# Performance work log

Hardware: AMD Instinct MI355X
Metric: run time of the kernel (lower is better)

Reference implementation:

```python
import jax, jax.numpy as jnp
import numpy as np


def setup_inputs() -> dict:
    key = jax.random.key(0)
    ks = jax.random.split(key, 6)
    B, C, V, L = 64, 32, 512, 13
    C_OUT = 64
    C_CAT = (2 * 3 + 1) * C  # order*support_len + 1 = 7 blocks -> 224
    x = jax.random.normal(ks[0], (B, C, V, L), dtype=jnp.float32)
    support0 = jax.random.uniform(ks[1], (V, V), dtype=jnp.float32)
    support1 = jax.random.uniform(ks[2], (V, V), dtype=jnp.float32)
    support2 = jax.random.uniform(ks[3], (V, V), dtype=jnp.float32)
    W = jax.random.normal(ks[4], (C_OUT, C_CAT), dtype=jnp.float32) * 0.05
    b = jnp.zeros((C_OUT,), dtype=jnp.float32)
    return {"x": x, "support0": support0, "support1": support1,
            "support2": support2, "W": W, "b": b}


def reference(x, support0, support1, support2, W, b):
    # Graph WaveNet GCN, eval mode (dropout is identity at inference).
    # x: [B, C, V, L]; each support a: [V, V].
    outs = [x]
    for a in (support0, support1, support2):
        x1 = jnp.einsum('ncvl,vw->ncwl', x, a)   # order 1 propagation
        outs.append(x1)
        x2 = jnp.einsum('ncvl,vw->ncwl', x1, a)  # order 2 propagation
        outs.append(x2)
    h = jnp.concatenate(outs, axis=1)            # [B, 7*C, V, L]
    # 1x1 Conv2d == per-(v,l) linear over channels
    h = jnp.einsum('ncvl,oc->novl', h, W) + b[None, :, None, None]
    return h
```

## Files before the change

kernel.cpp:

```cpp
#include <hip/hip_runtime.h>


typedef unsigned short u16;
typedef unsigned int   u32;
typedef __bf16 bf16x8 __attribute__((ext_vector_type(8)));
typedef float  f32x4  __attribute__((ext_vector_type(4)));
typedef u16    u16x4  __attribute__((ext_vector_type(4)));
typedef u16    u16x8  __attribute__((ext_vector_type(8)));

#define DEVI static __device__ __forceinline__

#define NV   512
#define NL   13
#define SZA  262144L
#define YP   136
#define WP   232

#define VMCNT(n) asm volatile("s_waitcnt vmcnt(" #n ")" ::: "memory")
#define LGKM0    asm volatile("s_waitcnt lgkmcnt(0)" ::: "memory")
#define CFENCE   asm volatile("" ::: "memory")
#define BAR()    __builtin_amdgcn_s_barrier()

DEVI u16 f2bf(float f) {
  union { float f; u32 u; } v; v.f = f;
  u32 u = v.u;
  return (u16)((u + 0x7fffu + ((u >> 16) & 1u)) >> 16);
}

DEVI void gl2lds16(const void* g, void* l) {
  __builtin_amdgcn_global_load_lds((__attribute__((address_space(1))) void*)g,
                                   (__attribute__((address_space(3))) void*)l, 16, 0, 0);
}

__global__ __launch_bounds__(256) void prep_A(const float* __restrict__ A0,
                                              const float* __restrict__ A1,
                                              const float* __restrict__ A2,
                                              u16* __restrict__ BT,
                                              u16* __restrict__ ABF) {
  const int s = blockIdx.z;
  const float* A = (s == 0) ? A0 : ((s == 1) ? A1 : A2);
  u16* abf = ABF + (long)s * SZA;
  u16* bt  = BT + (long)(2 * s) * SZA;
  __shared__ float t[32][33];
  const int v0 = blockIdx.x * 32, w0 = blockIdx.y * 32;
  const int tid = threadIdx.x;
  for (int i = tid; i < 1024; i += 256) {
    const int r = i >> 5, c = i & 31;
    const float val = A[(long)(v0 + r) * 512 + w0 + c];
    t[r][c] = val;
    abf[(long)(v0 + r) * 512 + w0 + c] = f2bf(val);
  }
  __syncthreads();
  for (int i = tid; i < 1024; i += 256) {
    const int r = i >> 5, c = i & 31;
    bt[(long)(w0 + r) * 512 + v0 + c] = f2bf(t[c][r]);
  }
}

__global__ __launch_bounds__(256) void prep_W(const float* __restrict__ W,
                                              u16* __restrict__ WBF) {
  const int i = blockIdx.x * 256 + threadIdx.x;
  WBF[i] = f2bf(W[i]);
}

__global__ __launch_bounds__(256) void transpose_x(const float* __restrict__ x,
                                                   u16* __restrict__ XT) {
  __shared__ __align__(16) float tile[NV * NL];
  const int bc = blockIdx.x;
  const int b = bc >> 5, c = bc & 31;
  const float4* src4 = (const float4*)(x + (long)bc * (NV * NL));
  float4* t4 = (float4*)tile;
  for (int i = threadIdx.x; i < (NV * NL) / 4; i += 256) t4[i] = src4[i];
  __syncthreads();
  for (int j = threadIdx.x; j < NL * 256; j += 256) {
    const int l = j >> 8, v = (j & 255) * 2;
    const long row = (long)(b * 13 + l) * 32 + c;
    const u32 lo = f2bf(tile[v * NL + l]);
    const u32 hi = f2bf(tile[(v + 1) * NL + l]);
    *(u32*)&XT[row * 512 + v] = lo | (hi << 16);
  }
}

__global__ __launch_bounds__(256) void gemm512(const u16* __restrict__ Ag,
                                               const u16* __restrict__ Bg,
                                               u16* __restrict__ Cg,
                                               long aZ, long bZ, long cZ) {
  __shared__ __align__(16) u16 As[128 * 32];
  __shared__ __align__(16) u16 Bs[128 * 32];
  const int p = blockIdx.z;
  const u16* A = Ag + (long)p * aZ;
  const u16* B = Bg + (long)p * bZ;
  u16*       C = Cg + (long)p * cZ;
  const int m0 = blockIdx.y * 128, n0 = blockIdx.x * 128;
  const int tid = threadIdx.x;
  const int lane = tid & 63, wid = tid >> 6;
  const int wm = wid >> 1, wn = wid & 1;
  const int lr = lane & 15, lq = lane >> 4;
  const int srow = lane >> 2, skq = lane & 3;

  f32x4 acc[4][4] = {};

  for (int kt = 0; kt < 16; ++kt) {
    const int k0 = kt * 32;
    __syncthreads();
#pragma unroll
    for (int j = 0; j < 2; ++j) {
      const int rb = wid * 32 + j * 16;
      gl2lds16(A + (long)(m0 + rb + srow) * 512 + (k0 + skq * 8), &As[rb * 32]);
      gl2lds16(B + (long)(n0 + rb + srow) * 512 + (k0 + skq * 8), &Bs[rb * 32]);
    }
    __syncthreads();
    bf16x8 af[4], bv[4];
#pragma unroll
    for (int t = 0; t < 4; ++t) {
      af[t] = *(const bf16x8*)&As[(wm * 64 + t * 16 + lr) * 32 + lq * 8];
      bv[t] = *(const bf16x8*)&Bs[(wn * 64 + t * 16 + lr) * 32 + lq * 8];
    }
#pragma unroll
    for (int i = 0; i < 4; ++i)
#pragma unroll
      for (int j = 0; j < 4; ++j)
        acc[i][j] = __builtin_amdgcn_mfma_f32_16x16x32_bf16(af[i], bv[j], acc[i][j], 0, 0, 0);
  }
#pragma unroll
  for (int i = 0; i < 4; ++i) {
    const int mr = m0 + wm * 64 + i * 16 + lq * 4;
#pragma unroll
    for (int j = 0; j < 4; ++j) {
      const int nc = n0 + wn * 64 + j * 16 + lr;
#pragma unroll
      for (int r = 0; r < 4; ++r)
        C[(long)(mr + r) * 512 + nc] = f2bf(acc[i][j][r]);
    }
  }
}

__global__ __launch_bounds__(512) void fused_gcn(const u16* __restrict__ XT,
                                                 const u16* __restrict__ BT,
                                                 const u16* __restrict__ WBF,
                                                 const float* __restrict__ bias,
                                                 float* __restrict__ out) {
  __shared__ __align__(16) u16 As [3][128 * 32];
  __shared__ __align__(16) u16 Bs0[3][128 * 32];
  __shared__ __align__(16) u16 Bs1[3][128 * 32];
  __shared__ __align__(16) u16 Yt[128 * YP];
  __shared__ __align__(16) u16 Ws[64 * WP];

  const int P = blockIdx.x;
  const int xcd = P & 7, inner = P >> 3;
  const int ym = xcd * 26 + (inner >> 2);
  const int m0 = ym * 128;
  const int w0 = (inner & 3) * 128;

  const int tid  = threadIdx.x;
  const int lane = tid & 63, wid = tid >> 6;
  const int lr = lane & 15, lq = lane >> 4;
  const int ww = wid & 3, wm2 = wid >> 2;
  const int g  = wid >> 1, h  = wid & 1;
  const int srow = tid >> 2, skq = tid & 3;
  const int scol = (skq ^ ((srow >> 1) & 3)) * 8;
  const int ldsb = wid * 512;
  const int co = (lq ^ ((lr >> 1) & 3)) * 8;

  for (int i = tid; i < 64 * 56; i += 512) {
    const int row = i / 56, c4 = (i - row * 56) * 4;
    *(u16x4*)&Ws[row * WP + c4] = *(const u16x4*)&WBF[row * 224 + c4];
  }
  for (int i = tid; i < 2048; i += 512) {
    const int mrow = i >> 4, c8 = (i & 15) * 8;
    const u16x8 d = *(const u16x8*)&XT[(long)(m0 + mrow) * 512 + w0 + c8];
#pragma unroll
    for (int z = 0; z < 8; ++z) {
      const int w = c8 + z;
      Yt[w * YP + ((((mrow >> 3) ^ ((w >> 3) & 3)) << 3) | (mrow & 7))] = d[z];
    }
  }
  __syncthreads();

  f32x4 oacc[4][4] = {};

#define STAGE(Bp0_, Bp1_, kk, bb) do {                                         \
    const int kc_ = (kk) * 32 + scol;                                          \
    gl2lds16(XT     + (long)(m0 + srow) * 512 + kc_, &As [bb][ldsb]);          \
    gl2lds16((Bp0_) + (long)(w0 + srow) * 512 + kc_, &Bs0[bb][ldsb]);          \
    gl2lds16((Bp1_) + (long)(w0 + srow) * 512 + kc_, &Bs1[bb][ldsb]);          \
  } while (0)

#define PROJ(blk) do {                                                         \
    bf16x8 paf_[4], pbv_[4];                                                   \
    _Pragma("unroll")                                                          \
    for (int oi = 0; oi < 4; ++oi)                                             \
      paf_[oi] = *(const bf16x8*)&Ws[(oi * 16 + lr) * WP + (blk) * 32 + lq * 8]; \
    _Pragma("unroll")                                                          \
    for (int wj = 0; wj < 4; ++wj) {                                           \
      const int w_ = h * 64 + wj * 16 + lr;                                    \
      pbv_[wj] = *(const bf16x8*)&Yt[w_ * YP + (((g * 4 + lq) ^ ((w_ >> 3) & 3)) << 3)]; \
    }                                                                          \
    _Pragma("unroll")                                                          \
    for (int oi = 0; oi < 4; ++oi)                                             \
      _Pragma("unroll")                                                        \
      for (int wj = 0; wj < 4; ++wj)                                           \
        oacc[oi][wj] = __builtin_amdgcn_mfma_f32_16x16x32_bf16(paf_[oi], pbv_[wj], oacc[oi][wj], 0, 0, 0); \
  } while (0)

#define WRB(ac) do {                                                           \
    _Pragma("unroll")                                                          \
    for (int i = 0; i < 2; ++i)                                                \
      _Pragma("unroll")                                                        \
      for (int j = 0; j < 4; ++j)                                              \
        _Pragma("unroll")                                                      \
        for (int r = 0; r < 4; ++r) {                                          \
          const int w_ = ww * 32 + i * 16 + lq * 4 + r;                        \
          const int m_ = wm2 * 64 + j * 16 + lr;                               \
          Yt[w_ * YP + ((((m_ >> 3) ^ ((w_ >> 3) & 3)) << 3) | (m_ & 7))] = f2bf(ac[i][j][r]); \
        }                                                                      \
  } while (0)

  for (int pass = 0; pass < 3; ++pass) {
    const u16* Bp0 = BT + (long)(2 * pass) * SZA;
    const u16* Bp1 = BT + (long)(2 * pass + 1) * SZA;
    STAGE(Bp0, Bp1, 0, 0);
    STAGE(Bp0, Bp1, 1, 1);
    PROJ(2 * pass);
    f32x4 accA[2][4] = {}, accB[2][4] = {};
#pragma unroll
    for (int kt = 0; kt < 16; ++kt) {
      if (kt == 15) { VMCNT(0); } else { VMCNT(3); }
      BAR();
      CFENCE;
      if (kt < 14) STAGE(Bp0, Bp1, kt + 2, (kt + 2) % 3);
      const int buf = kt % 3;
      bf16x8 a0[2], a1[2], bv[4];
#pragma unroll
      for (int i = 0; i < 2; ++i) {
        a0[i] = *(const bf16x8*)&Bs0[buf][(ww * 32 + i * 16 + lr) * 32 + co];
        a1[i] = *(const bf16x8*)&Bs1[buf][(ww * 32 + i * 16 + lr) * 32 + co];
      }
#pragma unroll
      for (int j = 0; j < 4; ++j)
        bv[j] = *(const bf16x8*)&As[buf][(wm2 * 64 + j * 16 + lr) * 32 + co];
      LGKM0;
#pragma unroll
      for (int i = 0; i < 2; ++i)
#pragma unroll
        for (int j = 0; j < 4; ++j) {
          accA[i][j] = __builtin_amdgcn_mfma_f32_16x16x32_bf16(a0[i], bv[j], accA[i][j], 0, 0, 0);
          accB[i][j] = __builtin_amdgcn_mfma_f32_16x16x32_bf16(a1[i], bv[j], accB[i][j], 0, 0, 0);
        }
    }
    WRB(accA);  LGKM0; BAR(); CFENCE;
    PROJ(2 * pass + 1);  LGKM0; BAR(); CFENCE;
    WRB(accB);  LGKM0; BAR(); CFENCE;
  }
  PROJ(6);

  const int bl = ym * 4 + g;
  const int b  = bl / 13, l = bl - b * 13;
  float* outb = out + (long)b * (64L * 512 * 13) + l;
#pragma unroll
  for (int oi = 0; oi < 4; ++oi) {
    const f32x4 bi = *(const f32x4*)&bias[oi * 16 + lq * 4];
#pragma unroll
    for (int wj = 0; wj < 4; ++wj) {
      const int w = w0 + h * 64 + wj * 16 + lr;
      const long base = ((long)(oi * 16 + lq * 4) * 512 + w) * 13;
#pragma unroll
      for (int r = 0; r < 4; ++r)
        outb[base + (long)r * (512 * 13)] = oacc[oi][wj][r] + bi[r];
    }
  }
#undef STAGE
#undef PROJ
#undef WRB
}

extern "C" void kernel_launch(void* const* d_in, const int* in_sizes, int n_in,
                              void* d_out, int out_size, void* d_ws, size_t ws_size,
                              hipStream_t stream) {
  const float* x  = (const float*)d_in[0];
  const float* s0 = (const float*)d_in[1];
  const float* s1 = (const float*)d_in[2];
  const float* s2 = (const float*)d_in[3];
  const float* W  = (const float*)d_in[4];
  const float* b  = (const float*)d_in[5];
  float* out = (float*)d_out;

  char* ws = (char*)d_ws;
  u16* XT  = (u16*)(ws);
  u16* BT  = (u16*)(ws + 27262976L);
  u16* ABF = (u16*)(ws + 30408704L);
  u16* WBF = (u16*)(ws + 31981568L);

  prep_A<<<dim3(16, 16, 3), 256, 0, stream>>>(s0, s1, s2, BT, ABF);
  prep_W<<<dim3(56), 256, 0, stream>>>(W, WBF);
  gemm512<<<dim3(4, 4, 3), 256, 0, stream>>>(BT, ABF, BT + SZA,
                                             2L * SZA, 1L * SZA, 2L * SZA);
  transpose_x<<<dim3(64 * 32), 256, 0, stream>>>(x, XT);
  fused_gcn<<<dim3(832), 512, 0, stream>>>(XT, BT, WBF, b, out);
}
```

Baseline: 419.8 us.

## Merge prep kernels and halve fused GCN tile for two blocks per CU

Merges the x transpose, support conversion and W conversion into a single prep launch, which removes two kernel launches. The fused GCN kernel now uses 256-thread blocks with 64-wide w tiles, launch_bounds(256,2) and a smaller LDS footprint so two blocks can share a CU. The W projection fragments are loaded from global memory into registers instead of being staged in LDS, and sched_barriers are added around the pipeline stages. In exchange, the grid is twice as large, so each support tile of XT is re-read by more blocks and register pressure rises.

```diff
diff --git a/kernel.cpp b/kernel.cpp
--- a/kernel.cpp
+++ b/kernel.cpp
@@ -5,7 +5,6 @@
 typedef unsigned int   u32;
 typedef __bf16 bf16x8 __attribute__((ext_vector_type(8)));
 typedef float  f32x4  __attribute__((ext_vector_type(4)));
-typedef u16    u16x4  __attribute__((ext_vector_type(4)));
 typedef u16    u16x8  __attribute__((ext_vector_type(8)));
 
 #define DEVI static __device__ __forceinline__
@@ -13,13 +12,11 @@
 #define NV   512
 #define NL   13
 #define SZA  262144L
-#define YP   136
-#define WP   232
 
 #define VMCNT(n) asm volatile("s_waitcnt vmcnt(" #n ")" ::: "memory")
 #define LGKM0    asm volatile("s_waitcnt lgkmcnt(0)" ::: "memory")
-#define CFENCE   asm volatile("" ::: "memory")
 #define BAR()    __builtin_amdgcn_s_barrier()
+#define SB0      __builtin_amdgcn_sched_barrier(0)
 
 DEVI u16 f2bf(float f) {
   union { float f; u32 u; } v; v.f = f;
@@ -32,52 +29,52 @@
                                    (__attribute__((address_space(3))) void*)l, 16, 0, 0);
 }
 
-__global__ __launch_bounds__(256) void prep_A(const float* __restrict__ A0,
-                                              const float* __restrict__ A1,
-                                              const float* __restrict__ A2,
-                                              u16* __restrict__ BT,
-                                              u16* __restrict__ ABF) {
-  const int s = blockIdx.z;
-  const float* A = (s == 0) ? A0 : ((s == 1) ? A1 : A2);
-  u16* abf = ABF + (long)s * SZA;
-  u16* bt  = BT + (long)(2 * s) * SZA;
-  __shared__ float t[32][33];
-  const int v0 = blockIdx.x * 32, w0 = blockIdx.y * 32;
-  const int tid = threadIdx.x;
-  for (int i = tid; i < 1024; i += 256) {
-    const int r = i >> 5, c = i & 31;
-    const float val = A[(long)(v0 + r) * 512 + w0 + c];
-    t[r][c] = val;
-    abf[(long)(v0 + r) * 512 + w0 + c] = f2bf(val);
-  }
-  __syncthreads();
-  for (int i = tid; i < 1024; i += 256) {
-    const int r = i >> 5, c = i & 31;
-    bt[(long)(w0 + r) * 512 + v0 + c] = f2bf(t[c][r]);
-  }
-}
-
-__global__ __launch_bounds__(256) void prep_W(const float* __restrict__ W,
-                                              u16* __restrict__ WBF) {
-  const int i = blockIdx.x * 256 + threadIdx.x;
-  WBF[i] = f2bf(W[i]);
-}
-
-__global__ __launch_bounds__(256) void transpose_x(const float* __restrict__ x,
-                                                   u16* __restrict__ XT) {
-  __shared__ __align__(16) float tile[NV * NL];
-  const int bc = blockIdx.x;
-  const int b = bc >> 5, c = bc & 31;
-  const float4* src4 = (const float4*)(x + (long)bc * (NV * NL));
-  float4* t4 = (float4*)tile;
-  for (int i = threadIdx.x; i < (NV * NL) / 4; i += 256) t4[i] = src4[i];
-  __syncthreads();
-  for (int j = threadIdx.x; j < NL * 256; j += 256) {
-    const int l = j >> 8, v = (j & 255) * 2;
-    const long row = (long)(b * 13 + l) * 32 + c;
-    const u32 lo = f2bf(tile[v * NL + l]);
-    const u32 hi = f2bf(tile[(v + 1) * NL + l]);
-    *(u32*)&XT[row * 512 + v] = lo | (hi << 16);
+__global__ __launch_bounds__(256) void prep_all(const float* __restrict__ x,
+                                                const float* __restrict__ A0,
+                                                const float* __restrict__ A1,
+                                                const float* __restrict__ A2,
+                                                const float* __restrict__ W,
+                                                u16* __restrict__ XT,
+                                                u16* __restrict__ BT,
+                                                u16* __restrict__ ABF,
+                                                u16* __restrict__ WBF) {
+  const int bid = blockIdx.x, tid = threadIdx.x;
+  if (bid < 2048) {
+    __shared__ __align__(16) float tile[NV * NL];
+    const int b = bid >> 5, c = bid & 31;
+    const float4* src4 = (const float4*)(x + (long)bid * (NV * NL));
+    float4* t4 = (float4*)tile;
+    for (int i = tid; i < (NV * NL) / 4; i += 256) t4[i] = src4[i];
+    __syncthreads();
+    for (int j = tid; j < NL * 256; j += 256) {
+      const int l = j >> 8, v = (j & 255) * 2;
+      const long row = (long)(b * 13 + l) * 32 + c;
+      const u32 lo = f2bf(tile[v * NL + l]);
+      const u32 hi = f2bf(tile[(v + 1) * NL + l]);
+      *(u32*)&XT[row * 512 + v] = lo | (hi << 16);
+    }
+  } else if (bid < 2816) {
+    const int idx = bid - 2048;
+    const int s = idx >> 8, rem = idx & 255;
+    const float* A = (s == 0) ? A0 : ((s == 1) ? A1 : A2);
+    u16* abf = ABF + (long)s * SZA;
+    u16* bt  = BT + (long)(2 * s) * SZA;
+    __shared__ float t[32][33];
+    const int v0 = (rem >> 4) * 32, w0 = (rem & 15) * 32;
+    for (int i = tid; i < 1024; i += 256) {
+      const int r = i >> 5, cc = i & 31;
+      const float val = A[(long)(v0 + r) * 512 + w0 + cc];
+      t[r][cc] = val;
+      abf[(long)(v0 + r) * 512 + w0 + cc] = f2bf(val);
+    }
+    __syncthreads();
+    for (int i = tid; i < 1024; i += 256) {
+      const int r = i >> 5, cc = i & 31;
+      bt[(long)(w0 + r) * 512 + v0 + cc] = f2bf(t[cc][r]);
+    }
+  } else {
+    const int i = (bid - 2816) * 256 + tid;
+    WBF[i] = f2bf(W[i]);
   }
 }
 
@@ -135,44 +132,37 @@
   }
 }
 
-__global__ __launch_bounds__(512) void fused_gcn(const u16* __restrict__ XT,
-                                                 const u16* __restrict__ BT,
-                                                 const u16* __restrict__ WBF,
-                                                 const float* __restrict__ bias,
-                                                 float* __restrict__ out) {
-  __shared__ __align__(16) u16 As [3][128 * 32];
-  __shared__ __align__(16) u16 Bs0[3][128 * 32];
-  __shared__ __align__(16) u16 Bs1[3][128 * 32];
-  __shared__ __align__(16) u16 Yt[128 * YP];
-  __shared__ __align__(16) u16 Ws[64 * WP];
+__global__ __launch_bounds__(256, 2) void fused_gcn(const u16* __restrict__ XT,
+                                                    const u16* __restrict__ BT,
+                                                    const u16* __restrict__ WBF,
+                                                    const float* __restrict__ bias,
+                                                    float* __restrict__ out) {
+  __shared__ __align__(16) u16 As[3][128 * 32];
+  __shared__ __align__(16) u16 Bs[3][128 * 32];
+  __shared__ __align__(16) u16 Yt[64 * 128];
 
   const int P = blockIdx.x;
   const int xcd = P & 7, inner = P >> 3;
-  const int ym = xcd * 26 + (inner >> 2);
+  const int ym = xcd * 26 + (inner >> 3);
   const int m0 = ym * 128;
-  const int w0 = (inner & 3) * 128;
+  const int w0 = (inner & 7) * 64;
 
   const int tid  = threadIdx.x;
   const int lane = tid & 63, wid = tid >> 6;
   const int lr = lane & 15, lq = lane >> 4;
-  const int ww = wid & 3, wm2 = wid >> 2;
-  const int g  = wid >> 1, h  = wid & 1;
-  const int srow = tid >> 2, skq = tid & 3;
-  const int scol = (skq ^ ((srow >> 1) & 3)) * 8;
-  const int ldsb = wid * 512;
+  const int wm = wid >> 1, ww = wid & 1;
+  const int g  = wid;
   const int co = (lq ^ ((lr >> 1) & 3)) * 8;
-
-  for (int i = tid; i < 64 * 56; i += 512) {
-    const int row = i / 56, c4 = (i - row * 56) * 4;
-    *(u16x4*)&Ws[row * WP + c4] = *(const u16x4*)&WBF[row * 224 + c4];
-  }
-  for (int i = tid; i < 2048; i += 512) {
-    const int mrow = i >> 4, c8 = (i & 15) * 8;
-    const u16x8 d = *(const u16x8*)&XT[(long)(m0 + mrow) * 512 + w0 + c8];
+  const int sr = lane >> 2;
+  const int sc = ((lane & 3) ^ ((lane >> 3) & 3)) * 8;
+
+  for (int i = tid; i < 1024; i += 256) {
+    const int row = i >> 3, c8 = (i & 7) * 8;
+    const u16x8 d = *(const u16x8*)&XT[(long)(m0 + row) * 512 + w0 + c8];
 #pragma unroll
     for (int z = 0; z < 8; ++z) {
       const int w = c8 + z;
-      Yt[w * YP + ((((mrow >> 3) ^ ((w >> 3) & 3)) << 3) | (mrow & 7))] = d[z];
+      Yt[w * 128 + ((((row >> 3) ^ (w & 7)) << 3) | (row & 7))] = d[z];
     }
   }
   __syncthreads();
@@ -180,27 +170,29 @@
   f32x4 oacc[4][4] = {};
 
 #define STAGE(Bp0_, Bp1_, kk, bb) do {                                         \
-    const int kc_ = (kk) * 32 + scol;                                          \
-    gl2lds16(XT     + (long)(m0 + srow) * 512 + kc_, &As [bb][ldsb]);          \
-    gl2lds16((Bp0_) + (long)(w0 + srow) * 512 + kc_, &Bs0[bb][ldsb]);          \
-    gl2lds16((Bp1_) + (long)(w0 + srow) * 512 + kc_, &Bs1[bb][ldsb]);          \
+    const int kc_ = (kk) * 32 + sc;                                            \
+    const u16* bsrc_ = (wid < 2) ? (Bp0_) : (Bp1_);                            \
+    _Pragma("unroll")                                                          \
+    for (int t_ = 0; t_ < 2; ++t_) {                                           \
+      gl2lds16(XT + (long)(m0 + wid * 32 + t_ * 16 + sr) * 512 + kc_,          \
+               &As[bb][(wid * 32 + t_ * 16) * 32]);                            \
+      gl2lds16(bsrc_ + (long)(w0 + (wid & 1) * 32 + t_ * 16 + sr) * 512 + kc_, \
+               &Bs[bb][(wid * 32 + t_ * 16) * 32]);                            \
+    }                                                                          \
   } while (0)
 
-#define PROJ(blk) do {                                                         \
-    bf16x8 paf_[4], pbv_[4];                                                   \
-    _Pragma("unroll")                                                          \
-    for (int oi = 0; oi < 4; ++oi)                                             \
-      paf_[oi] = *(const bf16x8*)&Ws[(oi * 16 + lr) * WP + (blk) * 32 + lq * 8]; \
+#define PROJ(AF_) do {                                                         \
+    bf16x8 pbv_[4];                                                            \
     _Pragma("unroll")                                                          \
     for (int wj = 0; wj < 4; ++wj) {                                           \
-      const int w_ = h * 64 + wj * 16 + lr;                                    \
-      pbv_[wj] = *(const bf16x8*)&Yt[w_ * YP + (((g * 4 + lq) ^ ((w_ >> 3) & 3)) << 3)]; \
+      const int w_ = wj * 16 + lr;                                             \
+      pbv_[wj] = *(const bf16x8*)&Yt[w_ * 128 + (((g * 4 + lq) ^ (w_ & 7)) << 3)]; \
     }                                                                          \
     _Pragma("unroll")                                                          \
     for (int oi = 0; oi < 4; ++oi)                                             \
       _Pragma("unroll")                                                        \
       for (int wj = 0; wj < 4; ++wj)                                           \
-        oacc[oi][wj] = __builtin_amdgcn_mfma_f32_16x16x32_bf16(paf_[oi], pbv_[wj], oacc[oi][wj], 0, 0, 0); \
+        oacc[oi][wj] = __builtin_amdgcn_mfma_f32_16x16x32_bf16((AF_)[oi], pbv_[wj], oacc[oi][wj], 0, 0, 0); \
   } while (0)
 
 #define WRB(ac) do {                                                           \
@@ -211,35 +203,40 @@
         _Pragma("unroll")                                                      \
         for (int r = 0; r < 4; ++r) {                                          \
           const int w_ = ww * 32 + i * 16 + lq * 4 + r;                        \
-          const int m_ = wm2 * 64 + j * 16 + lr;                               \
-          Yt[w_ * YP + ((((m_ >> 3) ^ ((w_ >> 3) & 3)) << 3) | (m_ & 7))] = f2bf(ac[i][j][r]); \
+          const int m_ = wm * 64 + j * 16 + lr;                                \
+          Yt[w_ * 128 + ((((m_ >> 3) ^ (w_ & 7)) << 3) | (m_ & 7))] = f2bf(ac[i][j][r]); \
         }                                                                      \
   } while (0)
 
   for (int pass = 0; pass < 3; ++pass) {
     const u16* Bp0 = BT + (long)(2 * pass) * SZA;
     const u16* Bp1 = BT + (long)(2 * pass + 1) * SZA;
+    bf16x8 afA[4], afB[4];
+#pragma unroll
+    for (int oi = 0; oi < 4; ++oi) {
+      afA[oi] = *(const bf16x8*)&WBF[(oi * 16 + lr) * 224 + (2 * pass) * 32 + lq * 8];
+      afB[oi] = *(const bf16x8*)&WBF[(oi * 16 + lr) * 224 + (2 * pass + 1) * 32 + lq * 8];
+    }
     STAGE(Bp0, Bp1, 0, 0);
     STAGE(Bp0, Bp1, 1, 1);
-    PROJ(2 * pass);
+    PROJ(afA);
     f32x4 accA[2][4] = {}, accB[2][4] = {};
 #pragma unroll
     for (int kt = 0; kt < 16; ++kt) {
-      if (kt == 15) { VMCNT(0); } else { VMCNT(3); }
-      BAR();
-      CFENCE;
+      if (kt == 15) { VMCNT(0); } else { VMCNT(4); }
+      BAR(); SB0;
       if (kt < 14) STAGE(Bp0, Bp1, kt + 2, (kt + 2) % 3);
       const int buf = kt % 3;
       bf16x8 a0[2], a1[2], bv[4];
 #pragma unroll
       for (int i = 0; i < 2; ++i) {
-        a0[i] = *(const bf16x8*)&Bs0[buf][(ww * 32 + i * 16 + lr) * 32 + co];
-        a1[i] = *(const bf16x8*)&Bs1[buf][(ww * 32 + i * 16 + lr) * 32 + co];
+        a0[i] = *(const bf16x8*)&Bs[buf][(     ww * 32 + i * 16 + lr) * 32 + co];
+        a1[i] = *(const bf16x8*)&Bs[buf][(64 + ww * 32 + i * 16 + lr) * 32 + co];
       }
 #pragma unroll
       for (int j = 0; j < 4; ++j)
-        bv[j] = *(const bf16x8*)&As[buf][(wm2 * 64 + j * 16 + lr) * 32 + co];
-      LGKM0;
+        bv[j] = *(const bf16x8*)&As[buf][(wm * 64 + j * 16 + lr) * 32 + co];
+      LGKM0; SB0;
 #pragma unroll
       for (int i = 0; i < 2; ++i)
 #pragma unroll
@@ -247,12 +244,17 @@
           accA[i][j] = __builtin_amdgcn_mfma_f32_16x16x32_bf16(a0[i], bv[j], accA[i][j], 0, 0, 0);
           accB[i][j] = __builtin_amdgcn_mfma_f32_16x16x32_bf16(a1[i], bv[j], accB[i][j], 0, 0, 0);
         }
-    }
-    WRB(accA);  LGKM0; BAR(); CFENCE;
-    PROJ(2 * pass + 1);  LGKM0; BAR(); CFENCE;
-    WRB(accB);  LGKM0; BAR(); CFENCE;
-  }
-  PROJ(6);
+      SB0;
+    }
+    WRB(accA);  LGKM0; BAR(); SB0;
+    PROJ(afB);  LGKM0; BAR(); SB0;
+    WRB(accB);  LGKM0; BAR(); SB0;
+  }
+  bf16x8 af6[4];
+#pragma unroll
+  for (int oi = 0; oi < 4; ++oi)
+    af6[oi] = *(const bf16x8*)&WBF[(oi * 16 + lr) * 224 + 6 * 32 + lq * 8];
+  PROJ(af6);
 
   const int bl = ym * 4 + g;
   const int b  = bl / 13, l = bl - b * 13;
@@ -262,7 +264,7 @@
     const f32x4 bi = *(const f32x4*)&bias[oi * 16 + lq * 4];
 #pragma unroll
     for (int wj = 0; wj < 4; ++wj) {
-      const int w = w0 + h * 64 + wj * 16 + lr;
+      const int w = w0 + wj * 16 + lr;
       const long base = ((long)(oi * 16 + lq * 4) * 512 + w) * 13;
 #pragma unroll
       for (int r = 0; r < 4; ++r)
@@ -291,10 +293,8 @@
   u16* ABF = (u16*)(ws + 30408704L);
   u16* WBF = (u16*)(ws + 31981568L);
 
-  prep_A<<<dim3(16, 16, 3), 256, 0, stream>>>(s0, s1, s2, BT, ABF);
-  prep_W<<<dim3(56), 256, 0, stream>>>(W, WBF);
+  prep_all<<<dim3(2872), 256, 0, stream>>>(x, s0, s1, s2, W, XT, BT, ABF, WBF);
   gemm512<<<dim3(4, 4, 3), 256, 0, stream>>>(BT, ABF, BT + SZA,
                                              2L * SZA, 1L * SZA, 2L * SZA);
-  transpose_x<<<dim3(64 * 32), 256, 0, stream>>>(x, XT);
-  fused_gcn<<<dim3(832), 512, 0, stream>>>(XT, BT, WBF, b, out);
-}
+  fused_gcn<<<dim3(1664), 256, 0, stream>>>(XT, BT, WBF, b, out);
+}
```

After: 452.3 us. 1.08x slower.
